# Optimization experiments

Measured on AMD Instinct MI355X. Metric: run time of the kernel, lower is better.

## Reference

```python
import jax, jax.numpy as jnp
import numpy as np
import math

D_MODEL = 1024
N_HEAD = 16
D_HEAD = D_MODEL // N_HEAD
B, T = 4, 2048


def setup_inputs() -> dict:
    key = jax.random.key(0)
    ks = jax.random.split(key, 9)
    x = jax.random.normal(ks[0], (B, T, D_MODEL), dtype=jnp.float32)
    # causal mask, broadcastable to [B, H, T, T]; mask==0 -> -1e9
    mask = jnp.tril(jnp.ones((T, T), dtype=bool))[None, None, :, :]
    # Xavier-uniform linear weights (stored as [in, out] for x @ W), zero biases
    limit = math.sqrt(6.0 / (D_MODEL + D_MODEL))
    def w(k):
        return jax.random.uniform(k, (D_MODEL, D_MODEL), dtype=jnp.float32, minval=-limit, maxval=limit)
    return {
        "x": x,
        "mask": mask,
        "wq": w(ks[1]), "bq": jnp.zeros((D_MODEL,), jnp.float32),
        "wk": w(ks[2]), "bk": jnp.zeros((D_MODEL,), jnp.float32),
        "wv": w(ks[3]), "bv": jnp.zeros((D_MODEL,), jnp.float32),
        "wo": w(ks[4]), "bo": jnp.zeros((D_MODEL,), jnp.float32),
    }


def reference(x, mask, wq, bq, wk, bk, wv, bv, wo, bo):
    b, t, c = x.shape
    h, dh = N_HEAD, D_HEAD
    # [B,T,C] -> [B,H,T,dh]
    def heads(y):
        return y.reshape(b, t, h, dh).transpose(0, 2, 1, 3)
    q = heads(x @ wq + bq)
    k = heads(x @ wk + bk)
    v = heads(x @ wv + bv)
    att = jnp.einsum("bhqd,bhkd->bhqk", q, k) / math.sqrt(dh)
    att = jnp.where(mask, att, jnp.float32(-1e9))
    att = jax.nn.softmax(att, axis=-1)  # dropout is identity in eval mode
    out = jnp.einsum("bhqk,bhkd->bhqd", att, v)
    out = out.transpose(0, 2, 1, 3).reshape(b, t, c)
    return out @ wo + bo
```

## Files before the change

kernel.cpp:

```cpp
#include <hip/hip_runtime.h>

typedef __bf16 bf16_t;
typedef bf16_t bf16x8 __attribute__((ext_vector_type(8)));
typedef bf16_t bf16x4 __attribute__((ext_vector_type(4)));
typedef float  f32x4  __attribute__((ext_vector_type(4)));
typedef float  f32x16 __attribute__((ext_vector_type(16)));
typedef unsigned int u32;
typedef u32 u32x2 __attribute__((ext_vector_type(2)));
typedef u32 u32x4 __attribute__((ext_vector_type(4)));

#define T_SEQ 2048
#define C_DIM 1024
#define NH    16
#define DH    64
#define BATCH 4
#define M_TOK (BATCH * T_SEQ)

#define Q_SCALE 0.1803368801111137f
#define DEFER_THR 8.0f

#define AS1 __attribute__((address_space(1)))
#define AS3 __attribute__((address_space(3)))

__device__ __forceinline__ void gld_lds16(const bf16_t* g, bf16_t* l) {
  __builtin_amdgcn_global_load_lds(
      (const AS1 u32*)(uintptr_t)g,
      (AS3 u32*)(u32)(uintptr_t)l, 16, 0, 0);
}

__device__ __forceinline__ void plswap(u32& a, u32& b) {
  u32x2 r = __builtin_amdgcn_permlane32_swap(a, b, false, false);
  a = r[0]; b = r[1];
}
__device__ __forceinline__ float xmax32(float x) {
  u32 a = __builtin_bit_cast(u32, x), b = a;
  plswap(a, b);
  return fmaxf(__builtin_bit_cast(float, a), __builtin_bit_cast(float, b));
}
__device__ __forceinline__ float xsum32(float x) {
  u32 a = __builtin_bit_cast(u32, x), b = a;
  plswap(a, b);
  return __builtin_bit_cast(float, a) + __builtin_bit_cast(float, b);
}

__device__ __forceinline__ u32 pack_bf16_pair(float v0, float v1) {
  const unsigned short b0 = __builtin_bit_cast(unsigned short, (bf16_t)v0);
  const unsigned short b1 = __builtin_bit_cast(unsigned short, (bf16_t)v1);
  return ((u32)b1 << 16) | (u32)b0;
}

__global__ __launch_bounds__(256) void msa_cvt_x(const float* __restrict__ x,
                                                 bf16_t* __restrict__ xb, int n4) {
  int i = blockIdx.x * 256 + threadIdx.x;
  if (i < n4) {
    const float4 v = ((const float4*)x)[i];
    bf16x4 o;
    o[0] = (bf16_t)v.x; o[1] = (bf16_t)v.y; o[2] = (bf16_t)v.z; o[3] = (bf16_t)v.w;
    ((bf16x4*)xb)[i] = o;
  }
}

__global__ __launch_bounds__(256) void msa_transpose_w(
    const float* __restrict__ wq, const float* __restrict__ wk,
    const float* __restrict__ wv, const float* __restrict__ wo,
    bf16_t* __restrict__ wt_qkv, bf16_t* __restrict__ wt_o) {
  __shared__ float tile[32][33];
  const int a = blockIdx.z;
  const float* src = (a == 0) ? wq : (a == 1) ? wk : (a == 2) ? wv : wo;
  bf16_t* dst = (a < 3) ? (wt_qkv + (size_t)a * C_DIM * C_DIM) : wt_o;
  const int tx = threadIdx.x & 31, ty = threadIdx.x >> 5;
  const int bi = blockIdx.y * 32, bj = blockIdx.x * 32;
#pragma unroll
  for (int p = 0; p < 4; p++) {
    int r = p * 8 + ty;
    tile[r][tx] = src[(size_t)(bi + r) * C_DIM + bj + tx];
  }
  __syncthreads();
#pragma unroll
  for (int p = 0; p < 4; p++) {
    int r = p * 8 + ty;
    dst[(size_t)(bj + r) * C_DIM + bi + tx] = (bf16_t)tile[tx][r];
  }
}

#define GQ_BUF 16384

#define GEMM_CORE(APTR, BPTR, NT)                                              \
  __shared__ __align__(16) char lds[3 * GQ_BUF];                               \
  const int tid = threadIdx.x;                                                 \
  const int w = tid >> 6, lane = tid & 63;                                     \
  const int lr = lane & 15, lg = lane >> 4;                                    \
  const int m0 = blockIdx.y * 128;                                             \
  const int n0 = blockIdx.x * 128;                                             \
  const int wm = (w >> 1) * 64, wn = (w & 1) * 64;                             \
  const int rsw = (lg * 16) ^ ((lr & 3) << 4);                                 \
  int Aoff[4], Boff[4];                                                        \
  _Pragma("unroll") for (int f = 0; f < 4; f++) {                              \
    Aoff[f] = (wm + f * 16 + lr) * 64 + rsw;                                   \
    Boff[f] = 8192 + (wn + f * 16 + lr) * 64 + rsw;                            \
  }                                                                            \
  const int idx0 = tid, idx1 = 256 + tid;                                      \
  const int r0 = idx0 >> 2, c0_ = ((idx0 & 3) ^ (r0 & 3)) * 8;                 \
  const int r1 = idx1 >> 2, c1_ = ((idx1 & 3) ^ (r1 & 3)) * 8;                 \
  const bf16_t* gA0 = (APTR) + (size_t)(m0 + r0) * C_DIM + c0_;                \
  const bf16_t* gA1 = (APTR) + (size_t)(m0 + r1) * C_DIM + c1_;                \
  const bf16_t* gB0 = (BPTR) + (size_t)(n0 + r0) * C_DIM + c0_;                \
  const bf16_t* gB1 = (BPTR) + (size_t)(n0 + r1) * C_DIM + c1_;                \
  f32x4 acc[4][4];                                                             \
  _Pragma("unroll") for (int i = 0; i < 4; i++)                                \
    _Pragma("unroll") for (int j = 0; j < 4; j++)                              \
      acc[i][j] = (f32x4){0.f, 0.f, 0.f, 0.f};                                 \
  GSTG(0, 0);                                                                  \
  GSTG(1, GQ_BUF);                                                             \
  asm volatile("s_waitcnt vmcnt(4)" ::: "memory");                             \
  __builtin_amdgcn_s_barrier();                                                \
  __builtin_amdgcn_sched_barrier(0);                                           \
  int cb = 0;                                                                  \
  for (int kt = 0; kt < (NT); ++kt) {                                          \
    const char* base = lds + cb * GQ_BUF;                                      \
    bf16x8 a[4], b[4];                                                         \
    _Pragma("unroll") for (int f = 0; f < 4; f++) {                            \
      a[f] = *(const bf16x8*)(base + Aoff[f]);                                 \
      b[f] = *(const bf16x8*)(base + Boff[f]);                                 \
    }                                                                          \
    if (kt < (NT)-2) {                                                         \
      int sb = cb + 2; if (sb >= 3) sb -= 3;                                   \
      GSTG(kt + 2, sb * GQ_BUF);                                               \
    }                                                                          \
    __builtin_amdgcn_s_setprio(1);                                             \
    _Pragma("unroll") for (int mf = 0; mf < 4; mf++)                           \
      _Pragma("unroll") for (int nf = 0; nf < 4; nf++)                         \
        acc[mf][nf] = __builtin_amdgcn_mfma_f32_16x16x32_bf16(                 \
            a[mf], b[nf], acc[mf][nf], 0, 0, 0);                               \
    __builtin_amdgcn_s_setprio(0);                                             \
    if (kt < (NT)-2) {                                                         \
      asm volatile("s_waitcnt vmcnt(4)" ::: "memory");                         \
    } else {                                                                   \
      asm volatile("s_waitcnt vmcnt(0)" ::: "memory");                         \
    }                                                                          \
    __builtin_amdgcn_s_barrier();                                              \
    __builtin_amdgcn_sched_barrier(0);                                         \
    if (++cb == 3) cb = 0;                                                     \
  }

#define GSTG(KT, BB)                                                           \
  {                                                                            \
    bf16_t* d_ = (bf16_t*)(lds + (BB));                                        \
    gld_lds16(gA0 + (KT) * 32, d_ + tid * 8);                                  \
    gld_lds16(gA1 + (KT) * 32, d_ + 2048 + tid * 8);                           \
    gld_lds16(gB0 + (KT) * 32, d_ + 4096 + tid * 8);                           \
    gld_lds16(gB1 + (KT) * 32, d_ + 6144 + tid * 8);                           \
  }

__global__ __launch_bounds__(256, 3) void msa_gemm_qkv(
    const bf16_t* __restrict__ xb, const bf16_t* __restrict__ wt,
    const float* __restrict__ bq, const float* __restrict__ bk,
    const float* __restrict__ bv,
    bf16_t* __restrict__ qo, bf16_t* __restrict__ ko, bf16_t* __restrict__ vto) {
  GEMM_CORE(xb, wt, 32)

  const int g = n0 >> 10;
  if (g == 2) {
#pragma unroll
    for (int nb = 0; nb < 4; nb++) {
      const int c = ((n0 + wn) & 1023) + nb * 16 + lr;
      const int h = c >> 6, d = c & 63;
      const float bias = bv[c];
      bf16_t* vrow = vto + (((size_t)((m0 >> 11) * NH + h)) * DH + d) * T_SEQ;
#pragma unroll
      for (int mb = 0; mb < 4; mb++) {
        const int t = (m0 & 2047) + wm + mb * 16 + lg * 4;
        u32x2 pr;
        pr[0] = pack_bf16_pair(acc[mb][nb][0] + bias, acc[mb][nb][1] + bias);
        pr[1] = pack_bf16_pair(acc[mb][nb][2] + bias, acc[mb][nb][3] + bias);
        *reinterpret_cast<u32x2*>(vrow + t) = pr;
      }
    }
  } else {
#pragma unroll
    for (int nb = 0; nb < 4; nb++) {
      const int n = n0 + wn + nb * 16 + lr;
      const int c = n & 1023, h = c >> 6, d = c & 63;
      const float bias = (g == 0) ? bq[c] : bk[c];
#pragma unroll
      for (int mb = 0; mb < 4; mb++) {
#pragma unroll
        for (int r = 0; r < 4; r++) {
          const int m = m0 + wm + mb * 16 + lg * 4 + r;
          const int bi = m >> 11, t = m & (T_SEQ - 1);
          float v = acc[mb][nb][r] + bias;
          if (g == 0)
            qo[(((size_t)bi * NH + h) * T_SEQ + t) * DH + d] = (bf16_t)(v * Q_SCALE);
          else
            ko[(((size_t)bi * NH + h) * T_SEQ + t) * DH + d] = (bf16_t)v;
        }
      }
    }
  }
}

__global__ __launch_bounds__(256, 3) void msa_gemm_out(
    const bf16_t* __restrict__ ab, const bf16_t* __restrict__ wt,
    const float* __restrict__ bo, float* __restrict__ out) {
  GEMM_CORE(ab, wt, 32)

#pragma unroll
  for (int nb = 0; nb < 4; nb++) {
    const int n = n0 + wn + nb * 16 + lr;
    const float bias = bo[n];
#pragma unroll
    for (int mb = 0; mb < 4; mb++) {
#pragma unroll
      for (int r = 0; r < 4; r++) {
        const int m = m0 + wm + mb * 16 + lg * 4 + r;
        out[(size_t)m * C_DIM + n] = acc[mb][nb][r] + bias;
      }
    }
  }
}

__device__ __forceinline__ void pack_frag(const f32x16& s, bf16x8& pa0, bf16x8& pa1) {
  u32 pk8[8];
#pragma unroll
  for (int i = 0; i < 8; i++) pk8[i] = pack_bf16_pair(s[2 * i], s[2 * i + 1]);
  u32 f0w0 = pk8[0], f0w2 = pk8[2];
  u32 f0w1 = pk8[1], f0w3 = pk8[3];
  u32 f1w0 = pk8[4], f1w2 = pk8[6];
  u32 f1w1 = pk8[5], f1w3 = pk8[7];
  plswap(f0w0, f0w2);
  plswap(f0w1, f0w3);
  plswap(f1w0, f1w2);
  plswap(f1w1, f1w3);
  const u32x4 q0v = {f0w0, f0w1, f0w2, f0w3};
  const u32x4 q1v = {f1w0, f1w1, f1w2, f1w3};
  pa0 = __builtin_bit_cast(bf16x8, q0v);
  pa1 = __builtin_bit_cast(bf16x8, q1v);
}

__device__ __forceinline__ void sm_pack(f32x16& s, float& m_run, float& l_run,
                                        f32x16& o0, f32x16& o1,
                                        bf16x8& pa0, bf16x8& pa1) {
  float t0 = fmaxf(fmaxf(s[0], s[1]), s[2]);
  float t1 = fmaxf(fmaxf(s[3], s[4]), s[5]);
  float t2 = fmaxf(fmaxf(s[6], s[7]), s[8]);
  float t3 = fmaxf(fmaxf(s[9], s[10]), s[11]);
  float t4 = fmaxf(fmaxf(s[12], s[13]), s[14]);
  float t5 = fmaxf(fmaxf(t0, t1), s[15]);
  float mt = fmaxf(fmaxf(fmaxf(t2, t3), t4), t5);
  mt = xmax32(mt);

  if (__any(mt > m_run + DEFER_THR)) {
    const float mnew = fmaxf(m_run, mt);
    const float al = __builtin_amdgcn_exp2f(m_run - mnew);
    m_run = mnew;
    l_run *= al;
#pragma unroll
    for (int r = 0; r < 16; r++) { o0[r] *= al; o1[r] *= al; }
  }

#pragma unroll
  for (int r = 0; r < 16; r++) s[r] = __builtin_amdgcn_exp2f(s[r] - m_run);
  {
    float a0 = (s[0] + s[1]) + (s[2] + s[3]);
    float a1 = (s[4] + s[5]) + (s[6] + s[7]);
    float a2 = (s[8] + s[9]) + (s[10] + s[11]);
    float a3 = (s[12] + s[13]) + (s[14] + s[15]);
    l_run += xsum32((a0 + a1) + (a2 + a3));
  }
  pack_frag(s, pa0, pa1);
}

__device__ __forceinline__ void store_o(f32x16& o0, f32x16& o1, float l_fin,
                                        bf16_t* __restrict__ orow, const int hi) {
  const float inv = 1.0f / l_fin;
#pragma unroll
  for (int db = 0; db < 2; db++) {
#pragma unroll
    for (int r = 0; r < 16; r += 2) {
      const int d = db * 32 + (r & 3) + 8 * (r >> 2) + 4 * hi;
      const float v0 = (db ? o1[r] : o0[r]) * inv;
      const float v1 = (db ? o1[r + 1] : o0[r + 1]) * inv;
      *reinterpret_cast<u32*>(orow + d) = pack_bf16_pair(v0, v1);
    }
  }
}

__global__ __launch_bounds__(256, 2) void msa_attn_lds(
    const bf16_t* __restrict__ Q, const bf16_t* __restrict__ K,
    const bf16_t* __restrict__ Vt, bf16_t* __restrict__ O) {
  __shared__ __align__(16) char lds[3 * 8192];
  const int tid = threadIdx.x;
  const int w = tid >> 6;
  const int lane = tid & 63;
  const int l31 = lane & 31;
  const int hi = lane >> 5;
  const int bh = blockIdx.x;
  const int pg = blockIdx.y;
  const int p = pg * 4 + w;
  const int tS = p, tL = 63 - p;
  const int q0S = tS * 32, q0L = tL * 32;
  const int KT_MAX = 63 - 4 * pg;

  const bf16_t* Qh = Q + (size_t)bh * T_SEQ * DH;
  const bf16_t* Kh = K + (size_t)bh * T_SEQ * DH;
  const bf16_t* Vh = Vt + (size_t)bh * DH * T_SEQ;

  bf16x8 qfL[4], qfS[4];
#pragma unroll
  for (int dc = 0; dc < 4; dc++) {
    qfL[dc] = *(const bf16x8*)(Qh + (size_t)(q0L + l31) * DH + dc * 16 + hi * 8);
    qfS[dc] = *(const bf16x8*)(Qh + (size_t)(q0S + l31) * DH + dc * 16 + hi * 8);
  }

  f32x16 oL0, oL1, oS0, oS1;
#pragma unroll
  for (int r = 0; r < 16; r++) { oL0[r] = 0.f; oL1[r] = 0.f; oS0[r] = 0.f; oS1[r] = 0.f; }
  float mL = -1e30f, lL = 0.f, mS = -1e30f, lS = 0.f;
  const f32x16 z16 = {};

  const int ksw = (l31 & 7) << 4;
  const int vsw = (l31 & 3) << 4;
  const int krow = tid >> 3;
  const int kce = ((16 * (tid & 7)) ^ ((krow & 7) << 4)) >> 1;
  const int vrow = tid >> 2;
  const int vce = ((16 * (tid & 3)) ^ ((vrow & 3) << 4)) >> 1;

#define STAGE(KT, BUF)                                                         \
  {                                                                            \
    const int jj = (KT) * 32;                                                  \
    bf16_t* base_ = (bf16_t*)(lds + (BUF) * 8192);                             \
    gld_lds16(Kh + (size_t)(jj + krow) * DH + kce, base_ + tid * 8);           \
    gld_lds16(Vh + (size_t)vrow * T_SEQ + jj + vce, base_ + 2048 + tid * 8);   \
  }

  STAGE(0, 0);
  STAGE(1, 1);
  asm volatile("s_waitcnt vmcnt(2)" ::: "memory");
  __builtin_amdgcn_s_barrier();
  __builtin_amdgcn_sched_barrier(0);

  int cb = 0;
  for (int kt = 0; kt <= KT_MAX; ++kt) {
    if (kt + 2 <= KT_MAX) {
      int sb = cb + 2; if (sb >= 3) sb -= 3;
      STAGE(kt + 2, sb);
    }

    const bool doL = (kt <= tL);
    if (doL) {
      const char* kb = lds + cb * 8192;
      const char* vb = kb + 4096;
      bf16x8 kf[4];
#pragma unroll
      for (int dc = 0; dc < 4; dc++)
        kf[dc] = *(const bf16x8*)(kb + l31 * 128 + ((dc * 32 + hi * 16) ^ ksw));
      const bf16x8 vf00 = *(const bf16x8*)(vb + l31 * 64 + ((hi * 16) ^ vsw));
      const bf16x8 vf01 = *(const bf16x8*)(vb + l31 * 64 + ((32 + hi * 16) ^ vsw));
      const bf16x8 vf10 = *(const bf16x8*)(vb + (32 + l31) * 64 + ((hi * 16) ^ vsw));
      const bf16x8 vf11 = *(const bf16x8*)(vb + (32 + l31) * 64 + ((32 + hi * 16) ^ vsw));

      const bool doS = (kt <= tS);
      f32x16 sL = __builtin_amdgcn_mfma_f32_32x32x16_bf16(kf[0], qfL[0], z16, 0, 0, 0);
#pragma unroll
      for (int dc = 1; dc < 4; dc++)
        sL = __builtin_amdgcn_mfma_f32_32x32x16_bf16(kf[dc], qfL[dc], sL, 0, 0, 0);
      f32x16 sS;
      if (doS) {
        sS = __builtin_amdgcn_mfma_f32_32x32x16_bf16(kf[0], qfS[0], z16, 0, 0, 0);
#pragma unroll
        for (int dc = 1; dc < 4; dc++)
          sS = __builtin_amdgcn_mfma_f32_32x32x16_bf16(kf[dc], qfS[dc], sS, 0, 0, 0);
      }
      if (kt == tL) {
#pragma unroll
        for (int r = 0; r < 16; r++) {
          const int jrow = (r & 3) + 8 * (r >> 2) + 4 * hi;
          if (jrow > l31) sL[r] = -1e30f;
        }
      }
      if (kt == tS) {
#pragma unroll
        for (int r = 0; r < 16; r++) {
          const int jrow = (r & 3) + 8 * (r >> 2) + 4 * hi;
          if (jrow > l31) sS[r] = -1e30f;
        }
      }
      bf16x8 paL0, paL1;
      sm_pack(sL, mL, lL, oL0, oL1, paL0, paL1);
      oL0 = __builtin_amdgcn_mfma_f32_32x32x16_bf16(vf00, paL0, oL0, 0, 0, 0);
      oL1 = __builtin_amdgcn_mfma_f32_32x32x16_bf16(vf10, paL0, oL1, 0, 0, 0);
      oL0 = __builtin_amdgcn_mfma_f32_32x32x16_bf16(vf01, paL1, oL0, 0, 0, 0);
      oL1 = __builtin_amdgcn_mfma_f32_32x32x16_bf16(vf11, paL1, oL1, 0, 0, 0);
      if (doS) {
        bf16x8 paS0, paS1;
        sm_pack(sS, mS, lS, oS0, oS1, paS0, paS1);
        oS0 = __builtin_amdgcn_mfma_f32_32x32x16_bf16(vf00, paS0, oS0, 0, 0, 0);
        oS1 = __builtin_amdgcn_mfma_f32_32x32x16_bf16(vf10, paS0, oS1, 0, 0, 0);
        oS0 = __builtin_amdgcn_mfma_f32_32x32x16_bf16(vf01, paS1, oS0, 0, 0, 0);
        oS1 = __builtin_amdgcn_mfma_f32_32x32x16_bf16(vf11, paS1, oS1, 0, 0, 0);
      }
    }

    if (kt < KT_MAX - 1) {
      asm volatile("s_waitcnt vmcnt(2)" ::: "memory");
    } else {
      asm volatile("s_waitcnt vmcnt(0)" ::: "memory");
    }
    __builtin_amdgcn_s_barrier();
    __builtin_amdgcn_sched_barrier(0);
    if (++cb == 3) cb = 0;
  }
#undef STAGE

  const int b = bh >> 4, h = bh & 15;
  store_o(oL0, oL1, lL, O + ((size_t)b * T_SEQ + q0L + l31) * C_DIM + h * DH, hi);
  store_o(oS0, oS1, lS, O + ((size_t)b * T_SEQ + q0S + l31) * C_DIM + h * DH, hi);
}

extern "C" void kernel_launch(void* const* d_in, const int* in_sizes, int n_in,
                              void* d_out, int out_size, void* d_ws, size_t ws_size,
                              hipStream_t stream) {
  const float* x  = (const float*)d_in[0];
  const float* wq = (const float*)d_in[2];
  const float* bq = (const float*)d_in[3];
  const float* wk = (const float*)d_in[4];
  const float* bk = (const float*)d_in[5];
  const float* wv = (const float*)d_in[6];
  const float* bv = (const float*)d_in[7];
  const float* wo = (const float*)d_in[8];
  const float* bo = (const float*)d_in[9];

  char* ws = (char*)d_ws;
  bf16_t* xb     = (bf16_t*)(ws);
  bf16_t* wt_qkv = (bf16_t*)(ws + (16ull << 20));
  bf16_t* wt_o   = (bf16_t*)(ws + (22ull << 20));
  bf16_t* qb     = (bf16_t*)(ws + (24ull << 20));
  bf16_t* kb     = (bf16_t*)(ws + (40ull << 20));
  bf16_t* vtb    = (bf16_t*)(ws + (56ull << 20));
  bf16_t* attn_o = xb;

  const int n4 = M_TOK * C_DIM / 4;
  msa_cvt_x<<<n4 / 256, 256, 0, stream>>>(x, xb, n4);
  msa_transpose_w<<<dim3(32, 32, 4), 256, 0, stream>>>(wq, wk, wv, wo, wt_qkv, wt_o);
  msa_gemm_qkv<<<dim3(24, 64), 256, 0, stream>>>(xb, wt_qkv, bq, bk, bv, qb, kb, vtb);
  msa_attn_lds<<<dim3(64, 8), 256, 0, stream>>>(qb, kb, vtb, attn_o);
  msa_gemm_out<<<dim3(8, 64), 256, 0, stream>>>(attn_o, wt_o, bo, (float*)d_out);
}
```

Before: 169.7 us.

## Enlarge GEMM tiles to 256x128 with 512 threads and fuse prep kernels

Both projection GEMMs move from 128x128 tiles on 256 threads to 256x128 tiles on 512 threads (8 waves). The aim is better reuse of each loaded B tile and fewer blocks; the LDS stage buffer grows to hold the larger A slice. Each thread now issues three staged loads per k-step, so the vmcnt waits change to match. The x conversion and weight transpose kernels are merged into one launch to save a kernel launch. The new launch_bounds(512,4) may cap registers tightly enough to cause spills of the 64-float accumulator, and the larger LDS footprint lowers occupancy.

```diff
diff --git a/kernel.cpp b/kernel.cpp
--- a/kernel.cpp
+++ b/kernel.cpp
@@ -49,70 +49,69 @@
   return ((u32)b1 << 16) | (u32)b0;
 }
 
-__global__ __launch_bounds__(256) void msa_cvt_x(const float* __restrict__ x,
-                                                 bf16_t* __restrict__ xb, int n4) {
-  int i = blockIdx.x * 256 + threadIdx.x;
-  if (i < n4) {
+__global__ __launch_bounds__(256) void msa_prep(
+    const float* __restrict__ x, bf16_t* __restrict__ xb,
+    const float* __restrict__ wq, const float* __restrict__ wk,
+    const float* __restrict__ wv, const float* __restrict__ wo,
+    bf16_t* __restrict__ wt_qkv, bf16_t* __restrict__ wt_o) {
+  __shared__ float tile[32][33];
+  const int blk = blockIdx.x;
+  if (blk < 8192) {
+    const int i = blk * 256 + threadIdx.x;
     const float4 v = ((const float4*)x)[i];
     bf16x4 o;
     o[0] = (bf16_t)v.x; o[1] = (bf16_t)v.y; o[2] = (bf16_t)v.z; o[3] = (bf16_t)v.w;
     ((bf16x4*)xb)[i] = o;
-  }
-}
-
-__global__ __launch_bounds__(256) void msa_transpose_w(
-    const float* __restrict__ wq, const float* __restrict__ wk,
-    const float* __restrict__ wv, const float* __restrict__ wo,
-    bf16_t* __restrict__ wt_qkv, bf16_t* __restrict__ wt_o) {
-  __shared__ float tile[32][33];
-  const int a = blockIdx.z;
-  const float* src = (a == 0) ? wq : (a == 1) ? wk : (a == 2) ? wv : wo;
-  bf16_t* dst = (a < 3) ? (wt_qkv + (size_t)a * C_DIM * C_DIM) : wt_o;
-  const int tx = threadIdx.x & 31, ty = threadIdx.x >> 5;
-  const int bi = blockIdx.y * 32, bj = blockIdx.x * 32;
-#pragma unroll
-  for (int p = 0; p < 4; p++) {
-    int r = p * 8 + ty;
-    tile[r][tx] = src[(size_t)(bi + r) * C_DIM + bj + tx];
-  }
-  __syncthreads();
-#pragma unroll
-  for (int p = 0; p < 4; p++) {
-    int r = p * 8 + ty;
-    dst[(size_t)(bj + r) * C_DIM + bi + tx] = (bf16_t)tile[tx][r];
-  }
-}
-
-#define GQ_BUF 16384
+  } else {
+    const int b2 = blk - 8192;
+    const int a = b2 >> 10;
+    const int bx = b2 & 31, by = (b2 >> 5) & 31;
+    const float* src = (a == 0) ? wq : (a == 1) ? wk : (a == 2) ? wv : wo;
+    bf16_t* dst = (a < 3) ? (wt_qkv + (size_t)a * C_DIM * C_DIM) : wt_o;
+    const int tx = threadIdx.x & 31, ty = threadIdx.x >> 5;
+    const int bi = by * 32, bj = bx * 32;
+#pragma unroll
+    for (int p = 0; p < 4; p++) {
+      int r = p * 8 + ty;
+      tile[r][tx] = src[(size_t)(bi + r) * C_DIM + bj + tx];
+    }
+    __syncthreads();
+#pragma unroll
+    for (int p = 0; p < 4; p++) {
+      int r = p * 8 + ty;
+      dst[(size_t)(bj + r) * C_DIM + bi + tx] = (bf16_t)tile[tx][r];
+    }
+  }
+}
+
+#define GQ_BUF 24576
 
 #define GEMM_CORE(APTR, BPTR, NT)                                              \
   __shared__ __align__(16) char lds[3 * GQ_BUF];                               \
   const int tid = threadIdx.x;                                                 \
   const int w = tid >> 6, lane = tid & 63;                                     \
   const int lr = lane & 15, lg = lane >> 4;                                    \
-  const int m0 = blockIdx.y * 128;                                             \
+  const int m0 = blockIdx.y * 256;                                             \
   const int n0 = blockIdx.x * 128;                                             \
   const int wm = (w >> 1) * 64, wn = (w & 1) * 64;                             \
   const int rsw = (lg * 16) ^ ((lr & 3) << 4);                                 \
   int Aoff[4], Boff[4];                                                        \
   _Pragma("unroll") for (int f = 0; f < 4; f++) {                              \
     Aoff[f] = (wm + f * 16 + lr) * 64 + rsw;                                   \
-    Boff[f] = 8192 + (wn + f * 16 + lr) * 64 + rsw;                            \
+    Boff[f] = 16384 + (wn + f * 16 + lr) * 64 + rsw;                           \
   }                                                                            \
-  const int idx0 = tid, idx1 = 256 + tid;                                      \
-  const int r0 = idx0 >> 2, c0_ = ((idx0 & 3) ^ (r0 & 3)) * 8;                 \
-  const int r1 = idx1 >> 2, c1_ = ((idx1 & 3) ^ (r1 & 3)) * 8;                 \
-  const bf16_t* gA0 = (APTR) + (size_t)(m0 + r0) * C_DIM + c0_;                \
-  const bf16_t* gA1 = (APTR) + (size_t)(m0 + r1) * C_DIM + c1_;                \
-  const bf16_t* gB0 = (BPTR) + (size_t)(n0 + r0) * C_DIM + c0_;                \
-  const bf16_t* gB1 = (BPTR) + (size_t)(n0 + r1) * C_DIM + c1_;                \
+  const int srow = tid >> 2;                                                   \
+  const int scol = (((tid & 3) ^ (srow & 3))) * 8;                             \
+  const bf16_t* gA0 = (APTR) + (size_t)(m0 + srow) * C_DIM + scol;             \
+  const bf16_t* gA1 = (APTR) + (size_t)(m0 + 128 + srow) * C_DIM + scol;       \
+  const bf16_t* gB0 = (BPTR) + (size_t)(n0 + srow) * C_DIM + scol;             \
   f32x4 acc[4][4];                                                             \
   _Pragma("unroll") for (int i = 0; i < 4; i++)                                \
     _Pragma("unroll") for (int j = 0; j < 4; j++)                              \
       acc[i][j] = (f32x4){0.f, 0.f, 0.f, 0.f};                                 \
   GSTG(0, 0);                                                                  \
   GSTG(1, GQ_BUF);                                                             \
-  asm volatile("s_waitcnt vmcnt(4)" ::: "memory");                             \
+  asm volatile("s_waitcnt vmcnt(3)" ::: "memory");                             \
   __builtin_amdgcn_s_barrier();                                                \
   __builtin_amdgcn_sched_barrier(0);                                           \
   int cb = 0;                                                                  \
@@ -134,7 +133,7 @@
             a[mf], b[nf], acc[mf][nf], 0, 0, 0);                               \
     __builtin_amdgcn_s_setprio(0);                                             \
     if (kt < (NT)-2) {                                                         \
-      asm volatile("s_waitcnt vmcnt(4)" ::: "memory");                         \
+      asm volatile("s_waitcnt vmcnt(3)" ::: "memory");                         \
     } else {                                                                   \
       asm volatile("s_waitcnt vmcnt(0)" ::: "memory");                         \
     }                                                                          \
@@ -147,12 +146,11 @@
   {                                                                            \
     bf16_t* d_ = (bf16_t*)(lds + (BB));                                        \
     gld_lds16(gA0 + (KT) * 32, d_ + tid * 8);                                  \
-    gld_lds16(gA1 + (KT) * 32, d_ + 2048 + tid * 8);                           \
-    gld_lds16(gB0 + (KT) * 32, d_ + 4096 + tid * 8);                           \
-    gld_lds16(gB1 + (KT) * 32, d_ + 6144 + tid * 8);                           \
-  }
-
-__global__ __launch_bounds__(256, 3) void msa_gemm_qkv(
+    gld_lds16(gA1 + (KT) * 32, d_ + 4096 + tid * 8);                           \
+    gld_lds16(gB0 + (KT) * 32, d_ + 8192 + tid * 8);                           \
+  }
+
+__global__ __launch_bounds__(512, 4) void msa_gemm_qkv(
     const bf16_t* __restrict__ xb, const bf16_t* __restrict__ wt,
     const float* __restrict__ bq, const float* __restrict__ bk,
     const float* __restrict__ bv,
@@ -199,7 +197,7 @@
   }
 }
 
-__global__ __launch_bounds__(256, 3) void msa_gemm_out(
+__global__ __launch_bounds__(512, 4) void msa_gemm_out(
     const bf16_t* __restrict__ ab, const bf16_t* __restrict__ wt,
     const float* __restrict__ bo, float* __restrict__ out) {
   GEMM_CORE(ab, wt, 32)
@@ -439,10 +437,8 @@
   bf16_t* vtb    = (bf16_t*)(ws + (56ull << 20));
   bf16_t* attn_o = xb;
 
-  const int n4 = M_TOK * C_DIM / 4;
-  msa_cvt_x<<<n4 / 256, 256, 0, stream>>>(x, xb, n4);
-  msa_transpose_w<<<dim3(32, 32, 4), 256, 0, stream>>>(wq, wk, wv, wo, wt_qkv, wt_o);
-  msa_gemm_qkv<<<dim3(24, 64), 256, 0, stream>>>(xb, wt_qkv, bq, bk, bv, qb, kb, vtb);
+  msa_prep<<<12288, 256, 0, stream>>>(x, xb, wq, wk, wv, wo, wt_qkv, wt_o);
+  msa_gemm_qkv<<<dim3(24, 32), 512, 0, stream>>>(xb, wt_qkv, bq, bk, bv, qb, kb, vtb);
   msa_attn_lds<<<dim3(64, 8), 256, 0, stream>>>(qb, kb, vtb, attn_o);
-  msa_gemm_out<<<dim3(8, 64), 256, 0, stream>>>(attn_o, wt_o, bo, (float*)d_out);
-}
+  msa_gemm_out<<<dim3(8, 32), 512, 0, stream>>>(attn_o, wt_o, bo, (float*)d_out);
+}
```

New measurement: 162.1 us. 1.05x faster.
